# Kernel tuning notes

Hardware: AMD Instinct MI355X
Metric: run time of the kernel (lower is better)

Reference implementation:

```python
import jax, jax.numpy as jnp
import numpy as np

N, C, H, W, HD = 32, 24, 12, 12, 128
GT, FP, A = 256, 256, 28
DIN = (C + 2) * 2 + HD  # 180, g_theta input dim


def setup_inputs() -> dict:
    key = jax.random.key(0)
    ks = jax.random.split(key, 18)
    def w(k, shape):
        fan_in = shape[0]
        return jax.random.normal(k, shape, jnp.float32) / np.sqrt(fan_in).astype(np.float32)
    inp = {
        "x": jax.random.normal(ks[0], (N, C, H, W), jnp.float32),
        "q": jax.random.normal(ks[1], (N, HD), jnp.float32),
        "gW0": w(ks[2], (DIN, GT)), "gb0": jnp.zeros((GT,), jnp.float32),
        "gW1": w(ks[3], (GT, GT)),  "gb1": jnp.zeros((GT,), jnp.float32),
        "gW2": w(ks[4], (GT, GT)),  "gb2": jnp.zeros((GT,), jnp.float32),
        "gW3": w(ks[5], (GT, GT)),  "gb3": jnp.zeros((GT,), jnp.float32),
        "fW0": w(ks[6], (GT, FP)),  "fb0": jnp.zeros((FP,), jnp.float32),
        "fW1": w(ks[7], (FP, FP)),  "fb1": jnp.zeros((FP,), jnp.float32),
        "fW2": w(ks[8], (FP, A)),   "fb2": jnp.zeros((A,), jnp.float32),
    }
    return inp


def _rn_forward(x, q, gW0, gb0, gW1, gb1, gW2, gb2, gW3, gb3,
                fW0, fb0, fW1, fb1, fW2, fb2):
    n, c, h, w = x.shape
    o = h * w
    # rn_encode: per-object features + (x, y) coordinates in [-1, 1]
    feats = x.reshape(n, c, o).transpose(0, 2, 1)            # [n, o, c]
    xc = jnp.repeat(jnp.linspace(-1.0, 1.0, h), w)           # row coord per pixel
    yc = jnp.tile(jnp.linspace(-1.0, 1.0, w), h)             # col coord per pixel
    coords = jnp.stack([xc, yc], axis=-1).astype(x.dtype)    # [o, 2]
    feats = jnp.concatenate([feats, jnp.broadcast_to(coords, (n, o, 2))], axis=-1)  # [n, o, c+2]
    cp = c + 2
    # pairs[n, a, b] = [feats[b], feats[a], q]  (matches torch unsqueeze(1)/unsqueeze(2))
    pairs = jnp.concatenate([
        jnp.broadcast_to(feats[:, None, :, :], (n, o, o, cp)),
        jnp.broadcast_to(feats[:, :, None, :], (n, o, o, cp)),
        jnp.broadcast_to(q[:, None, None, :], (n, o, o, q.shape[1])),
    ], axis=-1)                                              # [n, o, o, 2*cp+hd]
    # g_theta: 4-layer ReLU MLP applied per pair
    hdd = pairs
    for Wm, b in ((gW0, gb0), (gW1, gb1), (gW2, gb2), (gW3, gb3)):
        hdd = jax.nn.relu(jnp.einsum('nabd,de->nabe', hdd, Wm) + b)
    # lower_sum: keep lower-triangular (incl. diagonal) pairs, sum over them
    mask = jnp.tril(jnp.ones((o, o), hdd.dtype))[None, :, :, None]
    rel = jnp.sum(hdd * mask, axis=(1, 2))                   # [n, GT]
    # f_phi: ReLU hidden layers, linear output (dropout = eval mode no-op)
    y = jax.nn.relu(rel @ fW0 + fb0)
    y = jax.nn.relu(y @ fW1 + fb1)
    logits = y @ fW2 + fb2                                   # [n, A]
    return logits


def reference(x, q, gW0, gb0, gW1, gb1, gW2, gb2, gW3, gb3,
              fW0, fb0, fW1, fb1, fW2, fb2):
    return _rn_forward(x, q, gW0, gb0, gW1, gb1, gW2, gb2, gW3, gb3,
                       fW0, fb0, fW1, fb1, fW2, fb2)
```

## Files before the change

kernel.cpp:

```cpp
#include <hip/hip_runtime.h>
#include <hip/hip_bf16.h>

typedef __attribute__((ext_vector_type(8))) short short8;
typedef __attribute__((ext_vector_type(4))) short short4v;
typedef __attribute__((ext_vector_type(4))) float f32x4;

#define O 144
#define NB 32
#define GT 256
#define NPAIRS 10440
#define TP 128
#define NT 82

#define WS_WT   0u
#define WS_U    393216u
#define WS_V    2752512u
#define WS_REL  5144576u

#define SWZ(row, colb) ((colb) ^ (((row) & 7) << 4) ^ ((((colb) >> 2) & 0x60)))

__device__ __forceinline__ float bf2f(unsigned short b){
  unsigned int uu = ((unsigned int)b) << 16;
  return __builtin_bit_cast(float, uu);
}
__device__ __forceinline__ unsigned short f2bf(float f){
  unsigned int uu = __builtin_bit_cast(unsigned int, f);
  unsigned int lsb = (uu >> 16) & 1u;
  uu += 0x7fffu + lsb;
  return (unsigned short)(uu >> 16);
}

__global__ void prep_all(const float* __restrict__ x, const float* __restrict__ q,
                         const float* __restrict__ gW0, const float* __restrict__ gb0,
                         const float* __restrict__ gW1, const float* __restrict__ gW2,
                         const float* __restrict__ gW3,
                         unsigned short* __restrict__ u, unsigned short* __restrict__ v,
                         unsigned short* __restrict__ WtP, float* __restrict__ rel){
  int blk = blockIdx.x, t = threadIdx.x;
  if (blk < NB*O){
    int n = blk / O, o = blk - n*O;
    __shared__ float f[26];
    __shared__ float ql[128];
    if (t < 24) f[t] = x[(n*24 + t)*144 + o];
    if (t == 24) f[24] = -1.f + 2.f * (float)(o / 12) / 11.f;
    if (t == 25) f[25] = -1.f + 2.f * (float)(o % 12) / 11.f;
    if (t >= 128) ql[t - 128] = q[n*128 + (t - 128)];
    __syncthreads();
    float su = gb0[t], sv = 0.f;
    for (int d = 0; d < 128; d++) su += ql[d] * gW0[(52 + d)*GT + t];
    #pragma unroll
    for (int c = 0; c < 26; c++){
      float fc = f[c];
      su += fc * gW0[c*GT + t];
      sv += fc * gW0[(26 + c)*GT + t];
    }
    u[(size_t)(n*O + o)*GT + t] = f2bf(su);
    v[(size_t)(n*O + o)*GT + t] = f2bf(sv);
  } else {
    int b2 = blk - NB*O;
    int li = b2 >> 8, e = b2 & 255;
    const float* W = (li == 0) ? gW1 : (li == 1) ? gW2 : gW3;
    int et = e >> 4, r = e & 15;
    int kk = t >> 5, g = (t >> 3) & 3, d = t & 7;
    WtP[li*65536 + et*4096 + kk*512 + r*32 + g*8 + d] = f2bf(W[t*GT + e]);
    if (b2 < NB) rel[b2*GT + t] = 0.f;
  }
}

__global__ __launch_bounds__(256, 2) void rn_main(
    const unsigned short* __restrict__ u, const unsigned short* __restrict__ v,
    const unsigned short* __restrict__ WtP,
    const float* __restrict__ gb1, const float* __restrict__ gb2,
    const float* __restrict__ gb3, float* __restrict__ rel)
{
  __shared__ short8 hbuf[4096];
  char* lds = (char*)hbuf;

  const int tid  = threadIdx.x;
  const int lane = tid & 63;
  const int wav  = tid >> 6;
  const int n    = blockIdx.x / NT;
  const int tile = blockIdx.x - n*NT;
  const int tbase = tile * TP;
  const int l15 = lane & 15, l4 = lane >> 4;

  const unsigned short* wbase = WtP + wav*16384 + l15*32 + l4*8;
  short8 an0, an1, an2, an3;
#define LOADA(p_) { const unsigned short* _wp = wbase + ((p_) >> 3)*65536 + ((p_) & 7)*512; \
    an0 = *(const short8*)(_wp);         an1 = *(const short8*)(_wp + 4096);               \
    an2 = *(const short8*)(_wp + 8192);  an3 = *(const short8*)(_wp + 12288); }
  LOADA(0);

  {
    int row = wav*32 + (lane >> 1);
    int pt  = tbase + row;
    bool valid = pt < NPAIRS;
    int pa = 0, pb = 0;
    if (valid){
      pa = (int)((sqrtf(8.f*(float)pt + 1.f) - 1.f) * 0.5f);
      while ((pa + 1)*(pa + 2)/2 <= pt) pa++;
      while (pa*(pa + 1)/2 > pt) pa--;
      pb = pt - pa*(pa + 1)/2;
    }
    const unsigned short* up = u + (size_t)(n*O + pb)*GT;
    const unsigned short* vp = v + (size_t)(n*O + pa)*GT;
    int cbase = (lane & 1) * 128;
    #pragma unroll
    for (int cc = 0; cc < 16; cc++){
      int col = cbase + cc*8;
      short8 hv;
      if (valid){
        short8 uu = *(const short8*)(up + col);
        short8 vv = *(const short8*)(vp + col);
        #pragma unroll
        for (int j = 0; j < 8; j++){
          float s = bf2f((unsigned short)uu[j]) + bf2f((unsigned short)vv[j]);
          hv[j] = (short)f2bf(fmaxf(s, 0.f));
        }
      } else {
        #pragma unroll
        for (int j = 0; j < 8; j++) hv[j] = 0;
      }
      *(short8*)(lds + row*512 + SWZ(row, col*2)) = hv;
    }
  }
  __syncthreads();

  const bool fullvalid = (tbase + TP <= NPAIRS);
  f32x4 acc[4][8];

  #pragma unroll
  for (int L = 0; L < 3; L++){
    const float* gb = (L == 0) ? gb1 : (L == 1) ? gb2 : gb3;

    #pragma unroll
    for (int ie = 0; ie < 4; ie++){
      f32x4 bbv = *(const f32x4*)(gb + wav*64 + ie*16 + l4*4);
      #pragma unroll
      for (int jp = 0; jp < 8; jp++) acc[ie][jp] = bbv;
    }

    #pragma unroll
    for (int kk = 0; kk < 8; kk++){
      short8 a0 = an0, a1 = an1, a2 = an2, a3 = an3;
      int pn = L*8 + kk + 1; if (pn > 23) pn = 23;
      LOADA(pn);
      short8 b[8];
      #pragma unroll
      for (int jp = 0; jp < 8; jp++){
        int row = jp*16 + l15;
        b[jp] = *(short8*)(lds + row*512 + SWZ(row, kk*64 + l4*16));
      }
      #pragma unroll
      for (int jp = 0; jp < 8; jp++){
        acc[0][jp] = __builtin_amdgcn_mfma_f32_16x16x32_bf16(a0, b[jp], acc[0][jp], 0, 0, 0);
        acc[1][jp] = __builtin_amdgcn_mfma_f32_16x16x32_bf16(a1, b[jp], acc[1][jp], 0, 0, 0);
        acc[2][jp] = __builtin_amdgcn_mfma_f32_16x16x32_bf16(a2, b[jp], acc[2][jp], 0, 0, 0);
        acc[3][jp] = __builtin_amdgcn_mfma_f32_16x16x32_bf16(a3, b[jp], acc[3][jp], 0, 0, 0);
      }
    }

    if (L < 2){
      __syncthreads();
      #pragma unroll
      for (int ie = 0; ie < 4; ie++){
        int colb = (wav*64 + ie*16 + l4*4) * 2;
        #pragma unroll
        for (int jp = 0; jp < 8; jp++){
          int row = jp*16 + l15;
          short4v pk;
          #pragma unroll
          for (int j = 0; j < 4; j++)
            pk[j] = (short)f2bf(fmaxf(acc[ie][jp][j], 0.f));
          *(short4v*)(lds + row*512 + SWZ(row, colb)) = pk;
        }
      }
      __syncthreads();
    } else {
      #pragma unroll
      for (int ie = 0; ie < 4; ie++){
        int e0 = wav*64 + ie*16 + l4*4;
        f32x4 s = {0.f, 0.f, 0.f, 0.f};
        #pragma unroll
        for (int jp = 0; jp < 8; jp++){
          bool pv = fullvalid || (tbase + jp*16 + l15 < NPAIRS);
          #pragma unroll
          for (int j = 0; j < 4; j++){
            float hvv = fmaxf(acc[ie][jp][j], 0.f);
            s[j] += pv ? hvv : 0.f;
          }
        }
        #pragma unroll
        for (int st = 1; st < 16; st <<= 1){
          #pragma unroll
          for (int j = 0; j < 4; j++)
            s[j] += __shfl_xor(s[j], st);
        }
        if (l15 == 0){
          #pragma unroll
          for (int j = 0; j < 4; j++)
            atomicAdd(&rel[n*GT + e0 + j], s[j]);
        }
      }
    }
  }
#undef LOADA
}

__global__ void fphi(const float* __restrict__ rel,
                     const float* __restrict__ fW0, const float* __restrict__ fb0,
                     const float* __restrict__ fW1, const float* __restrict__ fb1,
                     const float* __restrict__ fW2, const float* __restrict__ fb2,
                     float* __restrict__ out){
  int n = blockIdx.x, t = threadIdx.x;
  __shared__ float h[256], y[256];
  h[t] = rel[n*GT + t];
  __syncthreads();
  float s = fb0[t];
  for (int k = 0; k < 256; k++) s += h[k] * fW0[k*GT + t];
  y[t] = fmaxf(s, 0.f);
  __syncthreads();
  s = fb1[t];
  for (int k = 0; k < 256; k++) s += y[k] * fW1[k*GT + t];
  __syncthreads();
  h[t] = fmaxf(s, 0.f);
  __syncthreads();
  if (t < 28){
    s = fb2[t];
    for (int k = 0; k < 256; k++) s += h[k] * fW2[k*28 + t];
    out[n*28 + t] = s;
  }
}

extern "C" void kernel_launch(void* const* d_in, const int* in_sizes, int n_in,
                              void* d_out, int out_size, void* d_ws, size_t ws_size,
                              hipStream_t stream){
  (void)in_sizes; (void)n_in; (void)out_size; (void)ws_size;
  const float* x   = (const float*)d_in[0];
  const float* q   = (const float*)d_in[1];
  const float* gW0 = (const float*)d_in[2];
  const float* gb0 = (const float*)d_in[3];
  const float* gW1 = (const float*)d_in[4];
  const float* gb1 = (const float*)d_in[5];
  const float* gW2 = (const float*)d_in[6];
  const float* gb2 = (const float*)d_in[7];
  const float* gW3 = (const float*)d_in[8];
  const float* gb3 = (const float*)d_in[9];
  const float* fW0 = (const float*)d_in[10];
  const float* fb0 = (const float*)d_in[11];
  const float* fW1 = (const float*)d_in[12];
  const float* fb1 = (const float*)d_in[13];
  const float* fW2 = (const float*)d_in[14];
  const float* fb2 = (const float*)d_in[15];

  char* ws = (char*)d_ws;
  unsigned short* WtP = (unsigned short*)(ws + WS_WT);
  unsigned short* u   = (unsigned short*)(ws + WS_U);
  unsigned short* v   = (unsigned short*)(ws + WS_V);
  float* rel = (float*)(ws + WS_REL);
  float* out = (float*)d_out;

  hipLaunchKernelGGL(prep_all, dim3(NB*O + 768), dim3(256), 0, stream,
                     x, q, gW0, gb0, gW1, gW2, gW3, u, v, WtP, rel);
  hipLaunchKernelGGL(rn_main, dim3(NB*NT), dim3(256), 0, stream,
                     u, v, WtP, gb1, gb2, gb3, rel);
  hipLaunchKernelGGL(fphi, dim3(NB), dim3(256), 0, stream,
                     rel, fW0, fb0, fW1, fb1, fW2, fb2, out);
}
```

Before: 297.2 us.

## Split prep kernel, amortize gW0 loads, simplify LDS swizzle, use packed bf16 converts

Splits the prep kernel into a u/v projection kernel and a weight-packing kernel. The projection kernel now handles 36 objects per block and keeps the gW0 columns and the query projection in registers, so they are not recomputed for every object. In the main kernel the LDS swizzle becomes a simpler precomputed XOR pattern, and the scalar bf16 rounding is replaced with v_cvt_pk_bf16_f32. s_setprio is also raised around the MFMA burst. The trade-offs are an extra kernel launch, fewer prep blocks with more serial work each, and possible changes in LDS bank-conflict behaviour.

```diff
diff --git a/kernel.cpp b/kernel.cpp
--- a/kernel.cpp
+++ b/kernel.cpp
@@ -2,7 +2,6 @@
 #include <hip/hip_bf16.h>
 
 typedef __attribute__((ext_vector_type(8))) short short8;
-typedef __attribute__((ext_vector_type(4))) short short4v;
 typedef __attribute__((ext_vector_type(4))) float f32x4;
 
 #define O 144
@@ -17,8 +16,6 @@
 #define WS_V    2752512u
 #define WS_REL  5144576u
 
-#define SWZ(row, colb) ((colb) ^ (((row) & 7) << 4) ^ ((((colb) >> 2) & 0x60)))
-
 __device__ __forceinline__ float bf2f(unsigned short b){
   unsigned int uu = ((unsigned int)b) << 16;
   return __builtin_bit_cast(float, uu);
@@ -29,42 +26,55 @@
   uu += 0x7fffu + lsb;
   return (unsigned short)(uu >> 16);
 }
-
-__global__ void prep_all(const float* __restrict__ x, const float* __restrict__ q,
-                         const float* __restrict__ gW0, const float* __restrict__ gb0,
-                         const float* __restrict__ gW1, const float* __restrict__ gW2,
-                         const float* __restrict__ gW3,
-                         unsigned short* __restrict__ u, unsigned short* __restrict__ v,
-                         unsigned short* __restrict__ WtP, float* __restrict__ rel){
-  int blk = blockIdx.x, t = threadIdx.x;
-  if (blk < NB*O){
-    int n = blk / O, o = blk - n*O;
-    __shared__ float f[26];
-    __shared__ float ql[128];
-    if (t < 24) f[t] = x[(n*24 + t)*144 + o];
-    if (t == 24) f[24] = -1.f + 2.f * (float)(o / 12) / 11.f;
-    if (t == 25) f[25] = -1.f + 2.f * (float)(o % 12) / 11.f;
-    if (t >= 128) ql[t - 128] = q[n*128 + (t - 128)];
-    __syncthreads();
-    float su = gb0[t], sv = 0.f;
-    for (int d = 0; d < 128; d++) su += ql[d] * gW0[(52 + d)*GT + t];
-    #pragma unroll
-    for (int c = 0; c < 26; c++){
-      float fc = f[c];
-      su += fc * gW0[c*GT + t];
-      sv += fc * gW0[(26 + c)*GT + t];
-    }
+__device__ __forceinline__ unsigned int cvtpk(float lo, float hi){
+  unsigned int r;
+  asm("v_cvt_pk_bf16_f32 %0, %1, %2" : "=v"(r) : "v"(lo), "v"(hi));
+  return r;
+}
+
+__global__ void prep_uv(const float* __restrict__ x, const float* __restrict__ q,
+                        const float* __restrict__ gW0, const float* __restrict__ gb0,
+                        unsigned short* __restrict__ u, unsigned short* __restrict__ v){
+  __shared__ float xs[24][36];
+  __shared__ float qs[128];
+  int n = blockIdx.x >> 2, oq = blockIdx.x & 3;
+  int t = threadIdx.x;
+  int o0 = oq * 36;
+  for (int i = t; i < 864; i += 256){
+    int c = i / 36, oo = i - c*36;
+    xs[c][oo] = x[(n*24 + c)*144 + o0 + oo];
+  }
+  if (t < 128) qs[t] = q[n*128 + t];
+  __syncthreads();
+  float wq = gb0[t];
+  for (int d = 0; d < 128; d++) wq += qs[d] * gW0[(52 + d)*GT + t];
+  float wc[52];
+  #pragma unroll
+  for (int c = 0; c < 52; c++) wc[c] = gW0[c*GT + t];
+  for (int oo = 0; oo < 36; oo++){
+    int o = o0 + oo;
+    float xc = -1.f + 2.f * (float)(o / 12) / 11.f;
+    float yc = -1.f + 2.f * (float)(o % 12) / 11.f;
+    float su = wq + xc*wc[24] + yc*wc[25];
+    float sv =      xc*wc[50] + yc*wc[51];
+    #pragma unroll
+    for (int c = 0; c < 24; c++){ float f = xs[c][oo]; su += f*wc[c]; sv += f*wc[26+c]; }
     u[(size_t)(n*O + o)*GT + t] = f2bf(su);
     v[(size_t)(n*O + o)*GT + t] = f2bf(sv);
-  } else {
-    int b2 = blk - NB*O;
-    int li = b2 >> 8, e = b2 & 255;
-    const float* W = (li == 0) ? gW1 : (li == 1) ? gW2 : gW3;
-    int et = e >> 4, r = e & 15;
-    int kk = t >> 5, g = (t >> 3) & 3, d = t & 7;
-    WtP[li*65536 + et*4096 + kk*512 + r*32 + g*8 + d] = f2bf(W[t*GT + e]);
-    if (b2 < NB) rel[b2*GT + t] = 0.f;
-  }
+  }
+}
+
+__global__ void prep_wt(const float* __restrict__ gW1, const float* __restrict__ gW2,
+                        const float* __restrict__ gW3, unsigned short* __restrict__ WtP,
+                        float* __restrict__ rel){
+  int li = blockIdx.x >> 8;
+  int e  = blockIdx.x & 255;
+  int k  = threadIdx.x;
+  const float* W = (li == 0) ? gW1 : (li == 1) ? gW2 : gW3;
+  int et = e >> 4, r = e & 15;
+  int kk = k >> 5, g = (k >> 3) & 3, d = k & 7;
+  WtP[li*65536 + et*4096 + kk*512 + r*32 + g*8 + d] = f2bf(W[k*GT + e]);
+  if (blockIdx.x < NB) rel[blockIdx.x*GT + k] = 0.f;
 }
 
 __global__ __launch_bounds__(256, 2) void rn_main(
@@ -102,31 +112,36 @@
       while (pa*(pa + 1)/2 > pt) pa--;
       pb = pt - pa*(pa + 1)/2;
     }
-    const unsigned short* up = u + (size_t)(n*O + pb)*GT;
-    const unsigned short* vp = v + (size_t)(n*O + pa)*GT;
-    int cbase = (lane & 1) * 128;
+    const uint4* up4 = (const uint4*)(u + (size_t)(n*O + pb)*GT);
+    const uint4* vp4 = (const uint4*)(v + (size_t)(n*O + pa)*GT);
+    int half = lane & 1;
+    int sbase = row*512 + half*256;
+    int ts = ((lane >> 1) & 3) << 4;
     #pragma unroll
     for (int cc = 0; cc < 16; cc++){
-      int col = cbase + cc*8;
-      short8 hv;
+      uint4 hv;
       if (valid){
-        short8 uu = *(const short8*)(up + col);
-        short8 vv = *(const short8*)(vp + col);
-        #pragma unroll
-        for (int j = 0; j < 8; j++){
-          float s = bf2f((unsigned short)uu[j]) + bf2f((unsigned short)vv[j]);
-          hv[j] = (short)f2bf(fmaxf(s, 0.f));
+        uint4 uu = up4[half*16 + cc];
+        uint4 vv = vp4[half*16 + cc];
+        #pragma unroll
+        for (int j = 0; j < 4; j++){
+          unsigned int ud = (&uu.x)[j], vd = (&vv.x)[j];
+          float lo = __builtin_bit_cast(float, ud << 16) + __builtin_bit_cast(float, vd << 16);
+          float hi = __builtin_bit_cast(float, ud & 0xffff0000u) + __builtin_bit_cast(float, vd & 0xffff0000u);
+          (&hv.x)[j] = cvtpk(fmaxf(lo, 0.f), fmaxf(hi, 0.f));
         }
       } else {
-        #pragma unroll
-        for (int j = 0; j < 8; j++) hv[j] = 0;
-      }
-      *(short8*)(lds + row*512 + SWZ(row, col*2)) = hv;
+        hv = (uint4){0u, 0u, 0u, 0u};
+      }
+      *(uint4*)(lds + sbase + ((cc*16) ^ ts)) = hv;
     }
   }
   __syncthreads();
 
   const bool fullvalid = (tbase + TP <= NPAIRS);
+  const int tsw = (l15 & 3) << 4;
+  const int rbase = l15*512 + ((l4*16) ^ tsw);
+  const int ebase = l15*512 + wav*128 + ((l4*8) ^ (tsw & 16));
   f32x4 acc[4][8];
 
   #pragma unroll
@@ -147,10 +162,9 @@
       LOADA(pn);
       short8 b[8];
       #pragma unroll
-      for (int jp = 0; jp < 8; jp++){
-        int row = jp*16 + l15;
-        b[jp] = *(short8*)(lds + row*512 + SWZ(row, kk*64 + l4*16));
-      }
+      for (int jp = 0; jp < 8; jp++)
+        b[jp] = *(short8*)(lds + rbase + jp*8192 + kk*64);
+      __builtin_amdgcn_s_setprio(1);
       #pragma unroll
       for (int jp = 0; jp < 8; jp++){
         acc[0][jp] = __builtin_amdgcn_mfma_f32_16x16x32_bf16(a0, b[jp], acc[0][jp], 0, 0, 0);
@@ -158,21 +172,20 @@
         acc[2][jp] = __builtin_amdgcn_mfma_f32_16x16x32_bf16(a2, b[jp], acc[2][jp], 0, 0, 0);
         acc[3][jp] = __builtin_amdgcn_mfma_f32_16x16x32_bf16(a3, b[jp], acc[3][jp], 0, 0, 0);
       }
+      __builtin_amdgcn_s_setprio(0);
     }
 
     if (L < 2){
       __syncthreads();
       #pragma unroll
       for (int ie = 0; ie < 4; ie++){
-        int colb = (wav*64 + ie*16 + l4*4) * 2;
+        int ea = ebase + ((ie*32) ^ (tsw & 32));
         #pragma unroll
         for (int jp = 0; jp < 8; jp++){
-          int row = jp*16 + l15;
-          short4v pk;
-          #pragma unroll
-          for (int j = 0; j < 4; j++)
-            pk[j] = (short)f2bf(fmaxf(acc[ie][jp][j], 0.f));
-          *(short4v*)(lds + row*512 + SWZ(row, colb)) = pk;
+          uint2 pk;
+          pk.x = cvtpk(fmaxf(acc[ie][jp][0], 0.f), fmaxf(acc[ie][jp][1], 0.f));
+          pk.y = cvtpk(fmaxf(acc[ie][jp][2], 0.f), fmaxf(acc[ie][jp][3], 0.f));
+          *(uint2*)(lds + ea + jp*8192) = pk;
         }
       }
       __syncthreads();
@@ -260,8 +273,8 @@
   float* rel = (float*)(ws + WS_REL);
   float* out = (float*)d_out;
 
-  hipLaunchKernelGGL(prep_all, dim3(NB*O + 768), dim3(256), 0, stream,
-                     x, q, gW0, gb0, gW1, gW2, gW3, u, v, WtP, rel);
+  hipLaunchKernelGGL(prep_uv, dim3(NB*4), dim3(256), 0, stream, x, q, gW0, gb0, u, v);
+  hipLaunchKernelGGL(prep_wt, dim3(768),  dim3(256), 0, stream, gW1, gW2, gW3, WtP, rel);
   hipLaunchKernelGGL(rn_main, dim3(NB*NT), dim3(256), 0, stream,
                      u, v, WtP, gb1, gb2, gb3, rel);
   hipLaunchKernelGGL(fphi, dim3(NB), dim3(256), 0, stream,
```

Measured after the change: 270.2 us. -9.1%, faster.
